# Performance work log

Hardware: AMD Instinct MI355X
Metric: run time of the kernel (lower is better)

The kernel has to match this reference:

```python
import jax, jax.numpy as jnp
import numpy as np

B, H, N, C, E, D, L_OUT, LAYERS = 16, 64, 512, 3, 128, 32, 12, 2


def setup_inputs() -> dict:
    key = jax.random.key(0)
    ks = jax.random.split(key, 16)
    nrm = lambda k, s, sc=1.0: jax.random.normal(k, s, jnp.float32) * sc
    adj = jax.random.uniform(ks[0], (N, N), jnp.float32)
    adj = adj / adj.sum(axis=-1, keepdims=True)  # row-normalized prior adjacency
    return {
        "x_input": nrm(ks[1], (B, H, N, C)),
        "adj": adj,
        "Wf": nrm(ks[2], (3, E, 3 * C), 0.1),
        "Uf": nrm(ks[3], (3, E, E), 0.05),
        "bf": jnp.zeros((3, E), jnp.float32),
        "E1f": nrm(ks[4], (N, D)),
        "E2f": nrm(ks[5], (N, D)),
        "Wb": nrm(ks[6], (3, E, 3 * C), 0.1),
        "Ub": nrm(ks[7], (3, E, E), 0.05),
        "bb": jnp.zeros((3, E), jnp.float32),
        "E1b": nrm(ks[8], (N, D)),
        "E2b": nrm(ks[9], (N, D)),
        "dec_w": nrm(ks[10], (L_OUT, LAYERS, 2 * E), 0.05),  # Conv2d(layer_num->out_len, k=(1,2E)) squeezed
        "dec_b": jnp.zeros((L_OUT,), jnp.float32),
        "out_w": nrm(ks[11], (L_OUT, L_OUT), 0.1),  # 1x1 Conv2d squeezed
        "out_b": jnp.zeros((L_OUT,), jnp.float32),
    }


def _cell_step(c, xt, adj, A_dyn, W, U, b):
    # Graph-coupled GRU cell (IBNCell): xt [B,C,N], c [B,E,N].
    msg = jnp.concatenate(
        [xt,
         jnp.einsum('bcn,nm->bcm', xt, adj),      # prior-graph message passing
         jnp.einsum('bcn,nm->bcm', xt, A_dyn)],   # learned dynamic-graph message passing
        axis=1)  # [B, 3C, N]
    gx = jnp.einsum('goc,bcn->gbon', W, msg)  # 3 stacked gate projections
    r = jax.nn.sigmoid(gx[0] + jnp.einsum('oe,ben->bon', U[0], c) + b[0][:, None])
    u = jax.nn.sigmoid(gx[1] + jnp.einsum('oe,ben->bon', U[1], c) + b[1][:, None])
    g = jnp.tanh(gx[2] + jnp.einsum('oe,ben->bon', U[2], r * c) + b[2][:, None])
    return u * c + (1.0 - u) * g


def _forward(x_input, adj, Wf, Uf, bf, E1f, E2f, Wb, Ub, bb, E1b, E2b, dec_w, dec_b, out_w, out_b):
    # torch: x_input.transpose(-3,-1).transpose(-2,-1) -> [B,C,H,N]; scan layout [H,B,C,N]
    xs = jnp.transpose(x_input, (1, 0, 3, 2))
    A_f = jax.nn.softmax(jax.nn.relu(E1f @ E2f.T), axis=-1)  # dynamic adjacency, fwd cell
    A_b = jax.nn.softmax(jax.nn.relu(E1b @ E2b.T), axis=-1)  # dynamic adjacency, back cell
    c0 = jnp.zeros((xs.shape[1], Wf.shape[1], xs.shape[3]), xs.dtype)  # [B,E,N]

    def step_f(c, xt):
        cn = _cell_step(c, xt, adj, A_f, Wf, Uf, bf)
        return cn, None

    # Output only depends on the last timestep of the bidirectional concat:
    # forward branch -> final state after H steps; backward branch (after flip)
    # at t=H-1 -> its FIRST step (input x[H-1]). Dead per-step outputs elided.
    h_fwd, _ = jax.lax.scan(step_f, c0, xs)
    h_back0 = _cell_step(c0, xs[-1], adj, A_b, Wb, Ub, bb)
    last_ht = jnp.concatenate([h_fwd, h_back0], axis=1)  # [B, 2E, N]

    lt = jnp.transpose(last_ht, (0, 2, 1))  # [B, N, 2E]
    # layer loop z>0 is a no-op on current_layer_output -> final_result repeats last_ht
    final = jnp.broadcast_to(lt[:, None], (lt.shape[0], LAYERS, lt.shape[1], lt.shape[2]))
    h = jnp.einsum('blne,ole->bon', final, dec_w) + dec_b[:, None]  # decoder conv (1,2E)
    return jnp.einsum('oi,bin->bon', out_w, h) + out_b[:, None]  # 1x1 output conv -> [B,L_OUT,N]


def reference(x_input, adj, Wf, Uf, bf, E1f, E2f, Wb, Ub, bb, E1b, E2b, dec_w, dec_b, out_w, out_b):
    return _forward(x_input, adj, Wf, Uf, bf, E1f, E2f, Wb, Ub, bb, E1b, E2b, dec_w, dec_b, out_w, out_b)
```

## Files before the change

### kernel.cpp

```cpp
#include <hip/hip_runtime.h>


typedef _Float16 half8_t __attribute__((ext_vector_type(8)));
typedef __fp16 fp16x2_t __attribute__((ext_vector_type(2)));
typedef float float4_t __attribute__((ext_vector_type(4)));

#define PIN(x) asm volatile("" : "+v"(x))

#define BAR_LDS()                                         \
  do {                                                    \
    asm volatile("s_waitcnt lgkmcnt(0)" ::: "memory");    \
    __builtin_amdgcn_s_barrier();                         \
  } while (0)

__device__ __forceinline__ float exp2_(float x) { return __builtin_amdgcn_exp2f(x); }
__device__ __forceinline__ float rcp_(float x) { return __builtin_amdgcn_rcpf(x); }

__global__ __launch_bounds__(256) void prep_kernel(
    const float* __restrict__ E1f, const float* __restrict__ E2f,
    const float* __restrict__ E1b, const float* __restrict__ E2b,
    const float* __restrict__ adj, const float* __restrict__ Wf,
    const float* __restrict__ Uf, const float* __restrict__ bf,
    const float* __restrict__ Wb, const float* __restrict__ bb,
    _Float16* __restrict__ adjT, _Float16* __restrict__ AfT,
    _Float16* __restrict__ AbT, _Float16* __restrict__ ufrag,
    _Float16* __restrict__ wbfrag, _Float16* __restrict__ zpad) {
  int bid = blockIdx.x;
  int tid = threadIdx.x;
  if (bid >= 1288) {
    if (tid < 64) zpad[tid] = (_Float16)0.f;
    return;
  }
  if (bid >= 1272) {
    int r2 = bid - 1272;
    int gi = 1 + (r2 & 1);
    int og = r2 >> 1;
    float scl = (gi == 2) ? 2.8853902f : -1.4426950f;
    for (int e = tid; e < 512; e += 256) {
      int lane = e >> 3, j = e & 7;
      int o = og * 16 + (lane & 15);
      int q = (lane >> 4) * 8 + j;
      float v = (q < 9) ? Wb[gi * 1152 + o * 9 + q]
                        : (q == 9 ? bb[gi * 128 + o] : 0.f);
      wbfrag[r2 * 512 + e] = (_Float16)(v * scl);
    }
    return;
  }
  if (bid >= 1152) {
    int r = bid - 1152;
    int kb = r % 5;
    int gi = (r / 5) % 3;
    int og = r / 15;
    float scl = (gi == 2) ? 2.8853902f : -1.4426950f;
    for (int e = tid; e < 512; e += 256) {
      int lane = e >> 3, j = e & 7;
      int o = og * 16 + (lane & 15);
      int q4 = lane >> 4;
      float v;
      if (kb < 4) {
        v = Uf[gi * 16384 + o * 128 + kb * 32 + q4 * 8 + j];
      } else {
        int q = q4 * 8 + j;
        v = (q < 9) ? Wf[gi * 1152 + o * 9 + q]
                    : (q == 9 ? bf[gi * 128 + o] : 0.f);
      }
      ufrag[r * 512 + e] = (_Float16)(v * scl);
    }
    return;
  }
  if (bid >= 1024) {
    int base = (bid - 1024) * 4;
    for (int r = 0; r < 4; ++r) {
      int row = base + r;
      float v0 = adj[row * 512 + tid];
      float v1 = adj[row * 512 + tid + 256];
      adjT[(size_t)tid * 512 + row] = (_Float16)v0;
      adjT[(size_t)(tid + 256) * 512 + row] = (_Float16)v1;
    }
    return;
  }
  int which = bid >> 9;
  int row = bid & 511;
  const float* E1 = which ? E1b : E1f;
  const float* E2 = which ? E2b : E2f;
  _Float16* A = which ? AbT : AfT;
  __shared__ float e1s[32];
  __shared__ float red[256];
  if (tid < 32) e1s[tid] = E1[row * 32 + tid];
  __syncthreads();
  float s[2];
#pragma unroll
  for (int h = 0; h < 2; ++h) {
    int m = tid + h * 256;
    const float4* e2 = (const float4*)(E2 + m * 32);
    float acc = 0.f;
#pragma unroll
    for (int d4 = 0; d4 < 8; ++d4) {
      float4 v = e2[d4];
      acc = fmaf(v.x, e1s[d4 * 4 + 0], acc);
      acc = fmaf(v.y, e1s[d4 * 4 + 1], acc);
      acc = fmaf(v.z, e1s[d4 * 4 + 2], acc);
      acc = fmaf(v.w, e1s[d4 * 4 + 3], acc);
    }
    s[h] = fmaxf(acc, 0.f);
  }
  red[tid] = fmaxf(s[0], s[1]);
  __syncthreads();
  for (int off = 128; off > 0; off >>= 1) {
    if (tid < off) red[tid] = fmaxf(red[tid], red[tid + off]);
    __syncthreads();
  }
  float mx = red[0];
  __syncthreads();
  float e0 = __expf(s[0] - mx), e1v = __expf(s[1] - mx);
  red[tid] = e0 + e1v;
  __syncthreads();
  for (int off = 128; off > 0; off >>= 1) {
    if (tid < off) red[tid] += red[tid + off];
    __syncthreads();
  }
  float inv = rcp_(red[0]);
  A[(size_t)tid * 512 + row] = (_Float16)(e0 * inv);
  A[(size_t)(tid + 256) * 512 + row] = (_Float16)(e1v * inv);
}

__global__ __launch_bounds__(256, 2) void msg_kernel(
    const float* __restrict__ x, const _Float16* __restrict__ adjT,
    const _Float16* __restrict__ AfT, const _Float16* __restrict__ AbT,
    _Float16* __restrict__ msg16, _Float16* __restrict__ msgb16) {
  __shared__ __align__(16) _Float16 Alds[48 * 512];
  __shared__ __align__(16) _Float16 Sst[1024 * 16];
  int tid = threadIdx.x;
  int t = blockIdx.x >> 3;
  int n0g = (blockIdx.x & 7) * 64;
  int lane = tid & 63, og = tid >> 6;
  int l15 = lane & 15, q4 = lane >> 4, q0 = q4 * 8;
  bool is63 = (t == 63);

  {
    union F24 { float4 v4[6]; float f[24]; };
    union P16 { fp16x2_t h2[4]; uint4 u; };
#pragma unroll
    for (int it = 0; it < 4; ++it) {
      int task = tid + it * 256;
      int b = task >> 6, chunk = task & 63;
      F24 fv;
      const float4* xb4 = (const float4*)x + ((size_t)(b * 64 + t) * 384 + chunk * 6);
#pragma unroll
      for (int i = 0; i < 6; ++i) fv.v4[i] = xb4[i];
#pragma unroll
      for (int c = 0; c < 3; ++c) {
        P16 p;
#pragma unroll
        for (int i = 0; i < 4; ++i)
          p.h2[i] = __builtin_amdgcn_cvt_pkrtz(fv.f[6 * i + c], fv.f[6 * i + 3 + c]);
        int m = b * 3 + c;
        *(uint4*)&Alds[m * 512 + ((chunk ^ (m & 7)) << 3)] = p.u;
      }
    }
  }
  __syncthreads();

  const float4_t zero4 = {0.f, 0.f, 0.f, 0.f};
  float4_t acc[3][2], accb[3];
#pragma unroll
  for (int mt = 0; mt < 3; ++mt) { acc[mt][0] = zero4; acc[mt][1] = zero4; accb[mt] = zero4; }

  int n = n0g + og * 16 + l15;
  for (int kb = 0; kb < 16; ++kb) {
    half8_t afr[3];
#pragma unroll
    for (int mt = 0; mt < 3; ++mt) {
      int m = mt * 16 + l15;
      afr[mt] = *(const half8_t*)&Alds[m * 512 + ((((kb * 4 + q4) ^ (m & 7)) << 3))];
    }
    half8_t b0 = *(const half8_t*)&adjT[(size_t)n * 512 + kb * 32 + q0];
    half8_t b1 = *(const half8_t*)&AfT[(size_t)n * 512 + kb * 32 + q0];
#pragma unroll
    for (int mt = 0; mt < 3; ++mt) {
      acc[mt][0] = __builtin_amdgcn_mfma_f32_16x16x32_f16(afr[mt], b0, acc[mt][0], 0, 0, 0);
      acc[mt][1] = __builtin_amdgcn_mfma_f32_16x16x32_f16(afr[mt], b1, acc[mt][1], 0, 0, 0);
    }
    if (is63) {
      half8_t b2 = *(const half8_t*)&AbT[(size_t)n * 512 + kb * 32 + q0];
#pragma unroll
      for (int mt = 0; mt < 3; ++mt)
        accb[mt] = __builtin_amdgcn_mfma_f32_16x16x32_f16(afr[mt], b2, accb[mt], 0, 0, 0);
    }
  }

  for (int i = tid; i < 1024; i += 256) {
    int tb = i >> 6, nl = i & 63;
    int nn = n0g + nl;
    _Float16* row = &Sst[i * 16];
#pragma unroll
    for (int c = 0; c < 3; ++c) {
      int m = tb * 3 + c;
      row[c] = Alds[m * 512 + ((((nn >> 3) ^ (m & 7)) << 3) | (nn & 7))];
    }
    row[9] = (_Float16)1.f;
#pragma unroll
    for (int z = 10; z < 16; ++z) row[z] = (_Float16)0.f;
  }
#pragma unroll
  for (int mt = 0; mt < 3; ++mt)
#pragma unroll
    for (int r = 0; r < 4; ++r) {
      int m = mt * 16 + q4 * 4 + r;
      int tb = (m * 21846) >> 16;
      int c = m - tb * 3;
      _Float16* row = &Sst[(tb * 64 + og * 16 + l15) * 16];
      row[3 + c] = (_Float16)acc[mt][0][r];
      row[6 + c] = (_Float16)acc[mt][1][r];
    }
  __syncthreads();
  for (int i = tid; i < 2048; i += 256) {
    int rrow = i >> 1, h = i & 1;
    int tb = rrow >> 6, nl = rrow & 63;
    ((uint4*)msg16)[(((size_t)(t * 16 + tb) * 512) + n0g + nl) * 2 + h] =
        ((const uint4*)Sst)[i];
  }
  if (is63) {
    __syncthreads();
#pragma unroll
    for (int mt = 0; mt < 3; ++mt)
#pragma unroll
      for (int r = 0; r < 4; ++r) {
        int m = mt * 16 + q4 * 4 + r;
        int tb = (m * 21846) >> 16;
        int c = m - tb * 3;
        Sst[(tb * 64 + og * 16 + l15) * 16 + 6 + c] = (_Float16)accb[mt][r];
      }
    __syncthreads();
    for (int i = tid; i < 2048; i += 256) {
      int rrow = i >> 1, h = i & 1;
      int tb = rrow >> 6, nl = rrow & 63;
      ((uint4*)msgb16)[(((size_t)tb * 512) + n0g + nl) * 2 + h] =
          ((const uint4*)Sst)[i];
    }
  }
}

__global__ __launch_bounds__(512, 4) void rec_kernel(
    const _Float16* __restrict__ msg16, const _Float16* __restrict__ msgb16,
    const _Float16* __restrict__ zpad, const _Float16* __restrict__ ufrag,
    const _Float16* __restrict__ wbfrag, const float* __restrict__ dec_w,
    const float* __restrict__ dec_b, const float* __restrict__ out_w,
    const float* __restrict__ out_b, float* __restrict__ out) {
  __shared__ __align__(16) _Float16 Cbuf[2048];
  __shared__ __align__(16) _Float16 Gbuf[2048];
  __shared__ float hf_lds[128 * 16];
  __shared__ float hb_lds[128 * 16];
  __shared__ float hdec_lds[12 * 16];
  int tid = threadIdx.x, bid = blockIdx.x;
  int b = bid >> 5;
  int nt = bid & 31;
  int n0 = nt * 16;
  int lane = tid & 63, og = tid >> 6;
  int l15 = lane & 15, q4 = lane >> 4;

  half8_t afrag[3][5];
#pragma unroll
  for (int gi = 0; gi < 3; ++gi)
#pragma unroll
    for (int kb = 0; kb < 5; ++kb) {
      afrag[gi][kb] = *(const half8_t*)
          &ufrag[(size_t)(((og * 3 + gi) * 5 + kb) * 512) + lane * 8];
      PIN(afrag[gi][kb]);
    }

  if (tid < 256) {
    uint4 z; z.x = z.y = z.z = z.w = 0;
    ((uint4*)Cbuf)[tid] = z;
  }
  float cr[4] = {0.f, 0.f, 0.f, 0.f};

  const float4_t zero4 = {0.f, 0.f, 0.f, 0.f};
  union H4U { fp16x2_t h2[2]; unsigned long long u; };
  const char* base = (const char*)msg16 +
                     ((size_t)(b * 512 + n0 + l15)) * 32 + (q4 & 1) * 16;
  const char* pcur = (q4 < 2) ? base : (const char*)zpad;
  size_t tstr = (q4 < 2) ? (size_t)16 * 512 * 32 : 0;
  half8_t bm = *(const half8_t*)pcur;

  float4_t accr_p = __builtin_amdgcn_mfma_f32_16x16x32_f16(afrag[0][4], bm, zero4, 0, 0, 0);

  int kb_w = og >> 1;
  int lane_w = ((og & 1) * 2 + (q4 >> 1)) * 16 + l15;
  int j0 = (q4 & 1) * 4;
  __syncthreads();

  for (int t = 0; t < 64; ++t) {
    const char* pnext = pcur + tstr;
    half8_t bm_n = *(const half8_t*)pnext;

    half8_t cf[4];
#pragma unroll
    for (int kb = 0; kb < 4; ++kb)
      cf[kb] = *(const half8_t*)&Cbuf[(kb * 64 + lane) * 8];

    float4_t accr = accr_p;
    __builtin_amdgcn_s_setprio(1);
#pragma unroll
    for (int kb = 0; kb < 4; ++kb)
      accr = __builtin_amdgcn_mfma_f32_16x16x32_f16(afrag[0][kb], cf[kb], accr, 0, 0, 0);
    __builtin_amdgcn_s_setprio(0);

    {
      H4U v;
#pragma unroll
      for (int r = 0; r < 2; ++r) {
        float a = rcp_(1.f + exp2_(accr[2 * r])) * cr[2 * r];
        float bq = rcp_(1.f + exp2_(accr[2 * r + 1])) * cr[2 * r + 1];
        v.h2[r] = __builtin_amdgcn_cvt_pkrtz(a, bq);
      }
      *(unsigned long long*)&Gbuf[(kb_w * 64 + lane_w) * 8 + j0] = v.u;
    }
    BAR_LDS();

    half8_t gf[4];
#pragma unroll
    for (int kb = 0; kb < 4; ++kb)
      gf[kb] = *(const half8_t*)&Gbuf[(kb * 64 + lane) * 8];
    __builtin_amdgcn_s_setprio(1);
    float4_t accu = __builtin_amdgcn_mfma_f32_16x16x32_f16(afrag[1][4], bm, zero4, 0, 0, 0);
#pragma unroll
    for (int kb = 0; kb < 4; ++kb)
      accu = __builtin_amdgcn_mfma_f32_16x16x32_f16(afrag[1][kb], cf[kb], accu, 0, 0, 0);
    float4_t accg = __builtin_amdgcn_mfma_f32_16x16x32_f16(afrag[2][4], bm, zero4, 0, 0, 0);
#pragma unroll
    for (int kb = 0; kb < 4; ++kb)
      accg = __builtin_amdgcn_mfma_f32_16x16x32_f16(afrag[2][kb], gf[kb], accg, 0, 0, 0);
    __builtin_amdgcn_s_setprio(0);

    {
      H4U v;
      float cn[4];
#pragma unroll
      for (int r = 0; r < 4; ++r) {
        float Eu = exp2_(accu[r]);
        float Eg = exp2_(accg[r]);
        float d0 = Eg + 1.f;
        float den = fmaf(Eu, d0, d0);
        float num = fmaf(cr[r], Eg, cr[r]) + fmaf(Eu, Eg, -Eu);
        cn[r] = num * rcp_(den);
        cr[r] = cn[r];
      }
      v.h2[0] = __builtin_amdgcn_cvt_pkrtz(cn[0], cn[1]);
      v.h2[1] = __builtin_amdgcn_cvt_pkrtz(cn[2], cn[3]);
      *(unsigned long long*)&Cbuf[(kb_w * 64 + lane_w) * 8 + j0] = v.u;
    }
    accr_p = __builtin_amdgcn_mfma_f32_16x16x32_f16(afrag[0][4], bm_n, zero4, 0, 0, 0);
    BAR_LDS();
    bm = bm_n;
    pcur = pnext;
  }

  {
    const char* bb_base = (const char*)msgb16 +
                          ((size_t)(b * 512 + n0 + l15)) * 32 + (q4 & 1) * 16;
    const char* bp = (q4 < 2) ? bb_base : (const char*)zpad;
    half8_t bbk = *(const half8_t*)bp;
    half8_t au_f = *(const half8_t*)&wbfrag[(size_t)((og * 2 + 0) * 512) + lane * 8];
    half8_t ag_f = *(const half8_t*)&wbfrag[(size_t)((og * 2 + 1) * 512) + lane * 8];
    float4_t au = __builtin_amdgcn_mfma_f32_16x16x32_f16(au_f, bbk, zero4, 0, 0, 0);
    float4_t ag = __builtin_amdgcn_mfma_f32_16x16x32_f16(ag_f, bbk, zero4, 0, 0, 0);
#pragma unroll
    for (int r = 0; r < 4; ++r) {
      int row = og * 16 + q4 * 4 + r;
      float uu2 = rcp_(1.f + exp2_(au[r]));
      float gg = fmaf(-2.f, rcp_(exp2_(ag[r]) + 1.f), 1.f);
      hb_lds[row * 16 + l15] = (1.f - uu2) * gg;
      hf_lds[row * 16 + l15] = cr[r];
    }
  }
  __syncthreads();

  if (tid < 192) {
    int i = tid >> 4, cc = tid & 15;
    const float* dwa = dec_w + (size_t)i * 512;
    const float* dwb = dwa + 256;
    float hd = dec_b[i];
    for (int e = 0; e < 128; ++e) {
      hd = fmaf(dwa[e] + dwb[e], hf_lds[e * 16 + cc], hd);
      hd = fmaf(dwa[128 + e] + dwb[128 + e], hb_lds[e * 16 + cc], hd);
    }
    hdec_lds[i * 16 + cc] = hd;
  }
  __syncthreads();
  if (tid < 192) {
    int o = tid >> 4, cc = tid & 15;
    float v = out_b[o];
#pragma unroll
    for (int i = 0; i < 12; ++i) v = fmaf(out_w[o * 12 + i], hdec_lds[i * 16 + cc], v);
    out[((size_t)(b * 12 + o)) * 512 + n0 + cc] = v;
  }
}

extern "C" void kernel_launch(void* const* d_in, const int* in_sizes, int n_in,
                              void* d_out, int out_size, void* d_ws, size_t ws_size,
                              hipStream_t stream) {
  (void)in_sizes; (void)n_in; (void)out_size; (void)ws_size;
  const float* x     = (const float*)d_in[0];
  const float* adj   = (const float*)d_in[1];
  const float* Wf    = (const float*)d_in[2];
  const float* Uf    = (const float*)d_in[3];
  const float* bf    = (const float*)d_in[4];
  const float* E1f   = (const float*)d_in[5];
  const float* E2f   = (const float*)d_in[6];
  const float* Wb    = (const float*)d_in[7];
  const float* bb    = (const float*)d_in[9];
  const float* E1b   = (const float*)d_in[10];
  const float* E2b   = (const float*)d_in[11];
  const float* dec_w = (const float*)d_in[12];
  const float* dec_b = (const float*)d_in[13];
  const float* out_w = (const float*)d_in[14];
  const float* out_b = (const float*)d_in[15];

  _Float16* h      = (_Float16*)d_ws;
  _Float16* adjT   = h;
  _Float16* AfT    = h + 262144;
  _Float16* AbT    = h + 524288;
  _Float16* ufrag  = h + 786432;
  _Float16* wbfrag = h + 847872;
  _Float16* zpad   = h + 856064;
  _Float16* msg16  = h + 856128;
  _Float16* msgb16 = h + 9244736;

  prep_kernel<<<1289, 256, 0, stream>>>(E1f, E2f, E1b, E2b, adj, Wf, Uf, bf,
                                        Wb, bb, adjT, AfT, AbT, ufrag, wbfrag, zpad);
  msg_kernel<<<512, 256, 0, stream>>>(x, adjT, AfT, AbT, msg16, msgb16);
  rec_kernel<<<512, 512, 0, stream>>>(msg16, msgb16, zpad, ufrag, wbfrag,
                                      dec_w, dec_b, out_w, out_b, (float*)d_out);
}
```

Before: 197.0 us.

## Pack two recurrence tiles per 1024-thread block with staggered barrier phases

Each block now runs two independent 16-node tiles, each on a 512-thread group with its own LDS buffers. Group 1 takes one extra barrier at the start and group 0 one at the end, so the groups run half a step apart on the shared block barriers. The aim is to overlap one group's MFMA phase with the other's exp/rcp gate math, hiding the serial latency of each recurrence step. The higher launch bounds (1024 threads, 4 blocks) may tighten the VGPR budget, which risks spilling the pinned weight fragments, and every barrier now couples 16 waves.

Result: no change. 197.2 us (+0.1%).

```diff
diff --git a/kernel.cpp b/kernel.cpp
--- a/kernel.cpp
+++ b/kernel.cpp
@@ -241,23 +241,27 @@
   }
 }
 
-__global__ __launch_bounds__(512, 4) void rec_kernel(
+__global__ __launch_bounds__(1024, 4) void rec_kernel(
     const _Float16* __restrict__ msg16, const _Float16* __restrict__ msgb16,
     const _Float16* __restrict__ zpad, const _Float16* __restrict__ ufrag,
     const _Float16* __restrict__ wbfrag, const float* __restrict__ dec_w,
     const float* __restrict__ dec_b, const float* __restrict__ out_w,
     const float* __restrict__ out_b, float* __restrict__ out) {
-  __shared__ __align__(16) _Float16 Cbuf[2048];
-  __shared__ __align__(16) _Float16 Gbuf[2048];
-  __shared__ float hf_lds[128 * 16];
-  __shared__ float hb_lds[128 * 16];
-  __shared__ float hdec_lds[12 * 16];
+  __shared__ __align__(16) _Float16 Cbuf2[2][2048];
+  __shared__ __align__(16) _Float16 Gbuf2[2][2048];
+  __shared__ float hf2[2][128 * 16];
+  __shared__ float hb2[2][128 * 16];
+  __shared__ float hdec2[2][192];
   int tid = threadIdx.x, bid = blockIdx.x;
-  int b = bid >> 5;
-  int nt = bid & 31;
-  int n0 = nt * 16;
-  int lane = tid & 63, og = tid >> 6;
+  int grp = tid >> 9;
+  int ltid = tid & 511;
+  int pid = (bid << 1) | grp;
+  int b = pid >> 5;
+  int n0 = (pid & 31) * 16;
+  int lane = ltid & 63, og = ltid >> 6;
   int l15 = lane & 15, q4 = lane >> 4;
+  _Float16* Cb = Cbuf2[grp];
+  _Float16* Gb = Gbuf2[grp];
 
   half8_t afrag[3][5];
 #pragma unroll
@@ -269,9 +273,9 @@
       PIN(afrag[gi][kb]);
     }
 
-  if (tid < 256) {
+  if (ltid < 256) {
     uint4 z; z.x = z.y = z.z = z.w = 0;
-    ((uint4*)Cbuf)[tid] = z;
+    ((uint4*)Cb)[ltid] = z;
   }
   float cr[4] = {0.f, 0.f, 0.f, 0.f};
 
@@ -289,6 +293,7 @@
   int lane_w = ((og & 1) * 2 + (q4 >> 1)) * 16 + l15;
   int j0 = (q4 & 1) * 4;
   __syncthreads();
+  if (grp) BAR_LDS();
 
   for (int t = 0; t < 64; ++t) {
     const char* pnext = pcur + tstr;
@@ -297,7 +302,7 @@
     half8_t cf[4];
 #pragma unroll
     for (int kb = 0; kb < 4; ++kb)
-      cf[kb] = *(const half8_t*)&Cbuf[(kb * 64 + lane) * 8];
+      cf[kb] = *(const half8_t*)&Cb[(kb * 64 + lane) * 8];
 
     float4_t accr = accr_p;
     __builtin_amdgcn_s_setprio(1);
@@ -314,14 +319,14 @@
         float bq = rcp_(1.f + exp2_(accr[2 * r + 1])) * cr[2 * r + 1];
         v.h2[r] = __builtin_amdgcn_cvt_pkrtz(a, bq);
       }
-      *(unsigned long long*)&Gbuf[(kb_w * 64 + lane_w) * 8 + j0] = v.u;
+      *(unsigned long long*)&Gb[(kb_w * 64 + lane_w) * 8 + j0] = v.u;
     }
     BAR_LDS();
 
     half8_t gf[4];
 #pragma unroll
     for (int kb = 0; kb < 4; ++kb)
-      gf[kb] = *(const half8_t*)&Gbuf[(kb * 64 + lane) * 8];
+      gf[kb] = *(const half8_t*)&Gb[(kb * 64 + lane) * 8];
     __builtin_amdgcn_s_setprio(1);
     float4_t accu = __builtin_amdgcn_mfma_f32_16x16x32_f16(afrag[1][4], bm, zero4, 0, 0, 0);
 #pragma unroll
@@ -348,13 +353,14 @@
       }
       v.h2[0] = __builtin_amdgcn_cvt_pkrtz(cn[0], cn[1]);
       v.h2[1] = __builtin_amdgcn_cvt_pkrtz(cn[2], cn[3]);
-      *(unsigned long long*)&Cbuf[(kb_w * 64 + lane_w) * 8 + j0] = v.u;
+      *(unsigned long long*)&Cb[(kb_w * 64 + lane_w) * 8 + j0] = v.u;
     }
     accr_p = __builtin_amdgcn_mfma_f32_16x16x32_f16(afrag[0][4], bm_n, zero4, 0, 0, 0);
     BAR_LDS();
     bm = bm_n;
     pcur = pnext;
   }
+  if (!grp) BAR_LDS();
 
   {
     const char* bb_base = (const char*)msgb16 +
@@ -370,29 +376,29 @@
       int row = og * 16 + q4 * 4 + r;
       float uu2 = rcp_(1.f + exp2_(au[r]));
       float gg = fmaf(-2.f, rcp_(exp2_(ag[r]) + 1.f), 1.f);
-      hb_lds[row * 16 + l15] = (1.f - uu2) * gg;
-      hf_lds[row * 16 + l15] = cr[r];
-    }
-  }
-  __syncthreads();
-
-  if (tid < 192) {
-    int i = tid >> 4, cc = tid & 15;
+      hb2[grp][row * 16 + l15] = (1.f - uu2) * gg;
+      hf2[grp][row * 16 + l15] = cr[r];
+    }
+  }
+  __syncthreads();
+
+  if (ltid < 192) {
+    int i = ltid >> 4, cc = ltid & 15;
     const float* dwa = dec_w + (size_t)i * 512;
     const float* dwb = dwa + 256;
     float hd = dec_b[i];
     for (int e = 0; e < 128; ++e) {
-      hd = fmaf(dwa[e] + dwb[e], hf_lds[e * 16 + cc], hd);
-      hd = fmaf(dwa[128 + e] + dwb[128 + e], hb_lds[e * 16 + cc], hd);
-    }
-    hdec_lds[i * 16 + cc] = hd;
-  }
-  __syncthreads();
-  if (tid < 192) {
-    int o = tid >> 4, cc = tid & 15;
+      hd = fmaf(dwa[e] + dwb[e], hf2[grp][e * 16 + cc], hd);
+      hd = fmaf(dwa[128 + e] + dwb[128 + e], hb2[grp][e * 16 + cc], hd);
+    }
+    hdec2[grp][i * 16 + cc] = hd;
+  }
+  __syncthreads();
+  if (ltid < 192) {
+    int o = ltid >> 4, cc = ltid & 15;
     float v = out_b[o];
 #pragma unroll
-    for (int i = 0; i < 12; ++i) v = fmaf(out_w[o * 12 + i], hdec_lds[i * 16 + cc], v);
+    for (int i = 0; i < 12; ++i) v = fmaf(out_w[o * 12 + i], hdec2[grp][i * 16 + cc], v);
     out[((size_t)(b * 12 + o)) * 512 + n0 + cc] = v;
   }
 }
@@ -430,6 +436,6 @@
   prep_kernel<<<1289, 256, 0, stream>>>(E1f, E2f, E1b, E2b, adj, Wf, Uf, bf,
                                         Wb, bb, adjT, AfT, AbT, ufrag, wbfrag, zpad);
   msg_kernel<<<512, 256, 0, stream>>>(x, adjT, AfT, AbT, msg16, msgb16);
-  rec_kernel<<<512, 512, 0, stream>>>(msg16, msgb16, zpad, ufrag, wbfrag,
-                                      dec_w, dec_b, out_w, out_b, (float*)d_out);
+  rec_kernel<<<256, 1024, 0, stream>>>(msg16, msgb16, zpad, ufrag, wbfrag,
+                                       dec_w, dec_b, out_w, out_b, (float*)d_out);
 }
```
